# Optimization experiments

Hardware: AMD Instinct MI355X
Metric: run time of the kernel (lower is better)

The kernel has to match this reference:

```python
import jax, jax.numpy as jnp
import numpy as np

DIM = 768
H = 12          # num_heads
KV = 4          # kv_heads
D = DIM // H    # head_dim = 64
ROPE_BASE = 10000.0
WINDOW = 8
B, N = 4, 1024


def setup_inputs() -> dict:
    key = jax.random.key(0)
    ks = jax.random.split(key, 8)
    s = 0.02  # weight scale for sane magnitudes
    return {
        "x": jax.random.normal(ks[0], (B, N, DIM), jnp.float32),
        "Wq": jax.random.normal(ks[1], (2 * DIM, DIM), jnp.float32) * s,
        "Wk": jax.random.normal(ks[2], (2 * DIM * KV // H, DIM), jnp.float32) * s,
        "Wv1": jax.random.normal(ks[3], (DIM * KV // H, DIM), jnp.float32) * s,
        "Wv2": jax.random.normal(ks[4], (DIM * KV // H, DIM), jnp.float32) * s,
        "lambda_p": jnp.full((H, 1, 1), -2.0, jnp.float32),
        "Wo": jax.random.normal(ks[5], (DIM, DIM), jnp.float32) * s,
        "bo": jax.random.normal(ks[6], (DIM,), jnp.float32) * s,
    }


def _rotate_half(x):
    x1 = x[..., ::2]
    x2 = x[..., 1::2]
    return jnp.stack([-x2, x1], axis=-1).reshape(x.shape)


def _rope_cos_sin(n, dtype):
    side = int(n ** 0.5)
    if side * side == n:
        h = np.arange(side, dtype=np.float32)
        gh, gw = np.meshgrid(h, h, indexing="ij")
        pos_h, pos_w = gh.reshape(-1), gw.reshape(-1)
    else:
        pos_h = np.arange(n, dtype=np.float32)
        pos_w = np.zeros_like(pos_h)
    dim_half = D // 2
    inv_freq = ROPE_BASE ** (-np.arange(dim_half, dtype=np.float32) / dim_half)
    theta = np.concatenate([pos_h[:, None] * inv_freq[None, :],
                            pos_w[:, None] * inv_freq[None, :]], axis=1)  # [N, D]
    cos = jnp.asarray(np.cos(theta), dtype)[None, None]  # [1,1,N,D]
    sin = jnp.asarray(np.sin(theta), dtype)[None, None]
    return cos, sin


def _apply_rope(q, cos, sin):
    return q * cos + _rotate_half(q) * sin


def _qk_norm(t):
    return t / (jnp.linalg.norm(t, axis=-1, keepdims=True) + 1e-6)


def _window_mask(n, dtype):
    side = int(n ** 0.5)
    if side * side == n:
        h = np.arange(side)
        gh, gw = np.meshgrid(h, h, indexing="ij")
        coords = np.stack([gh.reshape(-1), gw.reshape(-1)], axis=1)  # [N,2]
        dist = np.abs(coords[:, None, :] - coords[None, :, :]).max(-1)  # Chebyshev
    else:
        idx = np.arange(n)
        dist = np.abs(idx[None, :] - idx[:, None])
    return jnp.asarray(np.where(dist > WINDOW, -np.inf, 0.0).astype(np.float32), dtype)


def _attend(q, k, v, mask):
    # q,k,v: [B,H,N,D]; mask additive [N,N]
    scale = 1.0 / np.sqrt(D)
    scores = jnp.einsum("bhnd,bhmd->bhnm", q, k) * scale + mask
    return jnp.einsum("bhnm,bhmd->bhnd", jax.nn.softmax(scores, axis=-1), v)


def reference(x, Wq, Wk, Wv1, Wv2, lambda_p, Wo, bo):
    b, n, c = x.shape
    rep = H // KV
    q = (x @ Wq.T).reshape(b, n, 2, H, D).transpose(2, 0, 3, 1, 4)   # [2,B,H,N,D]
    k = (x @ Wk.T).reshape(b, n, 2, KV, D).transpose(2, 0, 3, 1, 4)  # [2,B,KV,N,D]
    v1 = (x @ Wv1.T).reshape(b, n, KV, D).transpose(0, 2, 1, 3)      # [B,KV,N,D]
    v2 = (x @ Wv2.T).reshape(b, n, KV, D).transpose(0, 2, 1, 3)
    q1, q2 = q[0], q[1]
    k1, k2 = k[0], k[1]
    # GQA: repeat_interleave over head axis
    k1 = jnp.repeat(k1, rep, axis=1)
    k2 = jnp.repeat(k2, rep, axis=1)
    v1 = jnp.repeat(v1, rep, axis=1)
    v2 = jnp.repeat(v2, rep, axis=1)
    cos, sin = _rope_cos_sin(n, x.dtype)
    q1, q2 = _apply_rope(q1, cos, sin), _apply_rope(q2, cos, sin)
    k1, k2 = _apply_rope(k1, cos, sin), _apply_rope(k2, cos, sin)
    q1, q2, k1, k2 = _qk_norm(q1), _qk_norm(q2), _qk_norm(k1), _qk_norm(k2)
    mask = _window_mask(n, x.dtype)
    out1 = _attend(q1, k1, v1, mask)
    out2 = _attend(q2, k2, v2, mask)
    lam = jax.nn.softplus(lambda_p)  # [H,1,1] broadcasts over [B,H,N,D]
    out = out1 - lam[None] * out2
    out = out.transpose(0, 2, 1, 3).reshape(b, n, c)
    return out @ Wo.T + bo
```

## Files before the change

### kernel.cpp

```cpp
#include <hip/hip_runtime.h>
#include <hip/hip_bf16.h>

#define BATCH 4
#define NSEQ  1024
#define DIM   768
#define NH    12
#define NKV   4
#define HD    64
#define NTOK  (BATCH*NSEQ)

using bf16 = __hip_bfloat16;
typedef __attribute__((ext_vector_type(8))) short short8;
typedef __attribute__((ext_vector_type(4))) float floatx4;

__device__ __forceinline__ float b2f(short x) {
  unsigned u = ((unsigned)(unsigned short)x) << 16;
  return __builtin_bit_cast(float, u);
}
__device__ __forceinline__ unsigned short f2b(float f) {
  unsigned u = __builtin_bit_cast(unsigned, f);
  unsigned r = u + 0x7FFF + ((u >> 16) & 1);
  return (unsigned short)(r >> 16);
}

__device__ __forceinline__ void load_lds_16(const bf16* g, bf16* l) {
  __builtin_amdgcn_global_load_lds(
      (const __attribute__((address_space(1))) void*)g,
      (__attribute__((address_space(3))) void*)l, 16, 0, 0);
}

__global__ __launch_bounds__(256) void cvt_all(
    const float* __restrict__ x,  const float* __restrict__ wq,
    const float* __restrict__ wk, const float* __restrict__ wv1,
    const float* __restrict__ wv2, const float* __restrict__ wo,
    bf16* __restrict__ xb,  bf16* __restrict__ wqb, bf16* __restrict__ wkb,
    bf16* __restrict__ wv1b, bf16* __restrict__ wv2b, bf16* __restrict__ wob)
{
  int i = blockIdx.x * 256 + threadIdx.x;
  const float* s; bf16* d; int off;
  if      (i <  786432) { s = x;   d = xb;   off = i; }
  else if (i < 1081344) { s = wq;  d = wqb;  off = i -  786432; }
  else if (i < 1179648) { s = wk;  d = wkb;  off = i - 1081344; }
  else if (i < 1228800) { s = wv1; d = wv1b; off = i - 1179648; }
  else if (i < 1277952) { s = wv2; d = wv2b; off = i - 1228800; }
  else                  { s = wo;  d = wob;  off = i - 1277952; }
  float4 f = reinterpret_cast<const float4*>(s)[off];
  ushort4 u;
  u.x = f2b(f.x); u.y = f2b(f.y); u.z = f2b(f.z); u.w = f2b(f.w);
  reinterpret_cast<ushort4*>(d)[off] = u;
}

__global__ __launch_bounds__(256, 2) void gemm_qkv(
    const bf16* __restrict__ xb,
    const bf16* __restrict__ Wqb, const bf16* __restrict__ Wkb,
    const bf16* __restrict__ Wv1b, const bf16* __restrict__ Wv2b,
    bf16* __restrict__ Qpk, bf16* __restrict__ Kpk,
    bf16* __restrict__ Vpk1, bf16* __restrict__ Vpk2)
{
  __shared__ __align__(16) bf16 As[128 * 32];
  __shared__ __align__(16) bf16 Ws[128 * 32];

  const int bn = blockIdx.x, bm = blockIdx.y;
  const bf16* Wp;
  if (bn < 12)      Wp = Wqb  + (size_t)bn * 128 * 768;
  else if (bn < 16) Wp = Wkb  + (size_t)(bn - 12) * 128 * 768;
  else if (bn < 18) Wp = Wv1b + (size_t)(bn - 16) * 128 * 768;
  else              Wp = Wv2b + (size_t)(bn - 18) * 128 * 768;

  const int t = threadIdx.x, wave = t >> 6, lane = t & 63;
  const int wm = wave >> 1, wn = wave & 1;
  const int quad = lane >> 4, lr = lane & 15;

  const int srow = wave * 32 + (lane >> 2);
  const int scol = (lane & 3) * 8;
  const bf16* Ag = xb + (size_t)(bm * 128 + srow) * 768 + scol;
  const bf16* Wg = Wp + (size_t)srow * 768 + scol;
  bf16* Al0 = As + wave * 1024;
  bf16* Al1 = As + wave * 1024 + 512;
  bf16* Wl0 = Ws + wave * 1024;
  bf16* Wl1 = Ws + wave * 1024 + 512;

  floatx4 acc[4][4] = {};

  for (int k0 = 0; k0 < 768; k0 += 32) {
    load_lds_16(Ag + k0,            Al0);
    load_lds_16(Ag + 16 * 768 + k0, Al1);
    load_lds_16(Wg + k0,            Wl0);
    load_lds_16(Wg + 16 * 768 + k0, Wl1);
    __syncthreads();

    short8 af[4], wf[4];
    #pragma unroll
    for (int mt = 0; mt < 4; ++mt)
      af[mt] = *reinterpret_cast<const short8*>(&As[(wm * 64 + mt * 16 + lr) * 32 + quad * 8]);
    #pragma unroll
    for (int nt = 0; nt < 4; ++nt)
      wf[nt] = *reinterpret_cast<const short8*>(&Ws[(wn * 64 + nt * 16 + lr) * 32 + quad * 8]);

    #pragma unroll
    for (int mt = 0; mt < 4; ++mt)
      #pragma unroll
      for (int nt = 0; nt < 4; ++nt)
        acc[mt][nt] = __builtin_amdgcn_mfma_f32_16x16x32_bf16(af[mt], wf[nt], acc[mt][nt], 0, 0, 0);
    __syncthreads();
  }

  if (bn < 16) {
    const float K2 = 0.41524101186098309f;
    const float invf0 = exp2f(-(float)lr * K2);
    const float invf1 = exp2f(-(float)(16 + lr) * K2);
    const float sgn = (lr & 1) ? 1.f : -1.f;
    const bool isq = (bn < 12);
    const int hq = bn * 2 + wn;
    const int sq_ = hq / 12, hq_ = hq % 12;
    const int hh = (bn - 12) * 2 + wn;
    const int sk_ = hh >> 2, kvh_ = hh & 3;
    const int qk128 = (lr >> 3) * 128;
    #pragma unroll
    for (int mt = 0; mt < 4; ++mt) {
      #pragma unroll
      for (int r = 0; r < 4; ++r) {
        int row = bm * 128 + wm * 64 + mt * 16 + quad * 4 + r;
        int n = row & (NSEQ - 1);
        float ph = (float)(n >> 5), pw = (float)(n & 31);
        float v0 = acc[mt][0][r];
        float v1 = acc[mt][1][r];
        float v2 = acc[mt][2][r];
        float v3 = acc[mt][3][r];
        float rot0 = sgn * __shfl_xor(v0, 1);
        float rot1 = sgn * __shfl_xor(v1, 1);
        float rot2 = sgn * __shfl_xor(v2, 1);
        float rot3 = sgn * __shfl_xor(v3, 1);
        float t0 = ph * invf0, t1 = ph * invf1, t2 = pw * invf0, t3 = pw * invf1;
        float rv0 = v0 * __cosf(t0) + rot0 * __sinf(t0);
        float rv1 = v1 * __cosf(t1) + rot1 * __sinf(t1);
        float rv2 = v2 * __cosf(t2) + rot2 * __sinf(t2);
        float rv3 = v3 * __cosf(t3) + rot3 * __sinf(t3);
        float ss = rv0 * rv0 + rv1 * rv1 + rv2 * rv2 + rv3 * rv3;
        #pragma unroll
        for (int off = 1; off < 16; off <<= 1) ss += __shfl_xor(ss, off);
        float sc = 1.f / (sqrtf(ss) + 1e-6f);
        int bb = row >> 10, kh = n >> 5;
        size_t fo = (size_t)(mt & 1) * 1024 + (quad * 4 + r) * 8 + (lr & 7) + qk128;
        bf16* tb;
        if (isq) {
          tb = Qpk + ((size_t)((bb * 2 + sq_) * 12 + hq_) * 32 + kh) * 2048 + fo;
        } else {
          tb = Kpk + ((size_t)((bb * 2 + sk_) * 4 + kvh_) * 32 + kh) * 2048 + fo;
        }
        *(unsigned short*)&tb[0]   = f2b(rv0 * sc);
        *(unsigned short*)&tb[256] = f2b(rv1 * sc);
        *(unsigned short*)&tb[512] = f2b(rv2 * sc);
        *(unsigned short*)&tb[768] = f2b(rv3 * sc);
      }
    }
  } else {
    const bool is2 = (bn >= 18);
    bf16* Vp = is2 ? Vpk2 : Vpk1;
    const int kvh_ = (bn - (is2 ? 18 : 16)) * 2 + wn;
    #pragma unroll
    for (int mt = 0; mt < 4; ++mt)
      #pragma unroll
      for (int r = 0; r < 4; ++r) {
        int row = bm * 128 + wm * 64 + mt * 16 + quad * 4 + r;
        int n = row & (NSEQ - 1);
        int bb = row >> 10, kh = n >> 5;
        int rowm = (mt & 1) * 16 + quad * 4 + r;
        int quad_v = rowm >> 3, j = rowm & 7;
        bf16* tb = Vp + ((size_t)(bb * 4 + kvh_) * 32 + kh) * 2048
                   + quad_v * 128 + lr * 8 + j;
        *(unsigned short*)&tb[0]    = f2b(acc[mt][0][r]);
        *(unsigned short*)&tb[512]  = f2b(acc[mt][1][r]);
        *(unsigned short*)&tb[1024] = f2b(acc[mt][2][r]);
        *(unsigned short*)&tb[1536] = f2b(acc[mt][3][r]);
      }
  }
}

__global__ __launch_bounds__(256) void gemm_out(
    const bf16* __restrict__ Xb, const bf16* __restrict__ Wob,
    float* __restrict__ out, const float* __restrict__ bias)
{
  __shared__ __align__(16) bf16 As[64 * 32];
  __shared__ __align__(16) bf16 Ws[64 * 32];

  const int bn = blockIdx.x, bm = blockIdx.y;
  const int t = threadIdx.x, wave = t >> 6, lane = t & 63;
  const int wm = wave >> 1, wn = wave & 1;
  const int quad = lane >> 4, lr = lane & 15;

  const int srow = wave * 16 + (lane >> 2);
  const int scol = (lane & 3) * 8;
  const bf16* Ag = Xb  + (size_t)(bm * 64 + srow) * 768 + scol;
  const bf16* Wg = Wob + (size_t)(bn * 64 + srow) * 768 + scol;
  bf16* Al = As + wave * 512;
  bf16* Wl = Ws + wave * 512;

  floatx4 acc[2][2] = {};

  for (int k0 = 0; k0 < 768; k0 += 32) {
    load_lds_16(Ag + k0, Al);
    load_lds_16(Wg + k0, Wl);
    __syncthreads();

    short8 af[2], wf[2];
    #pragma unroll
    for (int mt = 0; mt < 2; ++mt)
      af[mt] = *reinterpret_cast<const short8*>(&As[(wm * 32 + mt * 16 + lr) * 32 + quad * 8]);
    #pragma unroll
    for (int nt = 0; nt < 2; ++nt)
      wf[nt] = *reinterpret_cast<const short8*>(&Ws[(wn * 32 + nt * 16 + lr) * 32 + quad * 8]);

    #pragma unroll
    for (int mt = 0; mt < 2; ++mt)
      #pragma unroll
      for (int nt = 0; nt < 2; ++nt)
        acc[mt][nt] = __builtin_amdgcn_mfma_f32_16x16x32_bf16(af[mt], wf[nt], acc[mt][nt], 0, 0, 0);
    __syncthreads();
  }

  #pragma unroll
  for (int nt = 0; nt < 2; ++nt) {
    int col = bn * 64 + wn * 32 + nt * 16 + lr;
    float bv = bias[col];
    #pragma unroll
    for (int mt = 0; mt < 2; ++mt)
      #pragma unroll
      for (int r = 0; r < 4; ++r) {
        int row = bm * 64 + wm * 32 + mt * 16 + quad * 4 + r;
        out[(size_t)row * 768 + col] = acc[mt][nt][r] + bv;
      }
  }
}

struct Frag { short8 kf[2][2]; short8 vf[4]; };

__device__ __forceinline__ void attn_load(
    Frag& f, const bf16* __restrict__ kp, const bf16* __restrict__ vp,
    int kh, int lane8)
{
  const bf16* kt = kp + (size_t)kh * 2048 + lane8;
  const bf16* vt = vp + (size_t)kh * 2048 + lane8;
  f.kf[0][0] = *reinterpret_cast<const short8*>(kt);
  f.kf[0][1] = *reinterpret_cast<const short8*>(kt + 512);
  f.kf[1][0] = *reinterpret_cast<const short8*>(kt + 1024);
  f.kf[1][1] = *reinterpret_cast<const short8*>(kt + 1536);
  f.vf[0] = *reinterpret_cast<const short8*>(vt);
  f.vf[1] = *reinterpret_cast<const short8*>(vt + 512);
  f.vf[2] = *reinterpret_cast<const short8*>(vt + 1024);
  f.vf[3] = *reinterpret_cast<const short8*>(vt + 1536);
}

__device__ __forceinline__ void attn_step(
    const short8 (&qf)[2][2], const Frag& f, unsigned maskbits,
    floatx4 (&O)[2][4], float (&psum)[2][4], bf16* __restrict__ Pl,
    int quad, int lr)
{
  floatx4 S[2][2] = {};
  #pragma unroll
  for (int ks = 0; ks < 2; ++ks) {
    S[0][0] = __builtin_amdgcn_mfma_f32_16x16x32_bf16(qf[0][ks], f.kf[0][ks], S[0][0], 0, 0, 0);
    S[0][1] = __builtin_amdgcn_mfma_f32_16x16x32_bf16(qf[0][ks], f.kf[1][ks], S[0][1], 0, 0, 0);
    S[1][0] = __builtin_amdgcn_mfma_f32_16x16x32_bf16(qf[1][ks], f.kf[0][ks], S[1][0], 0, 0, 0);
    S[1][1] = __builtin_amdgcn_mfma_f32_16x16x32_bf16(qf[1][ks], f.kf[1][ks], S[1][1], 0, 0, 0);
  }

  #pragma unroll
  for (int mt = 0; mt < 2; ++mt)
    #pragma unroll
    for (int nt = 0; nt < 2; ++nt)
      #pragma unroll
      for (int r = 0; r < 4; ++r) {
        float p = __expf(S[mt][nt][r] * 0.125f);
        p = ((maskbits >> (mt * 8 + nt * 4 + r)) & 1u) ? p : 0.0f;
        psum[mt][r] += p;
        *(unsigned short*)&Pl[(mt * 16 + quad * 4 + r) * 40 + nt * 16 + lr] = f2b(p);
      }

  short8 pf0 = *reinterpret_cast<const short8*>(&Pl[(lr) * 40 + quad * 8]);
  short8 pf1 = *reinterpret_cast<const short8*>(&Pl[(16 + lr) * 40 + quad * 8]);
  #pragma unroll
  for (int ntd = 0; ntd < 4; ++ntd) {
    O[0][ntd] = __builtin_amdgcn_mfma_f32_16x16x32_bf16(pf0, f.vf[ntd], O[0][ntd], 0, 0, 0);
    O[1][ntd] = __builtin_amdgcn_mfma_f32_16x16x32_bf16(pf1, f.vf[ntd], O[1][ntd], 0, 0, 0);
  }
}

__global__ __launch_bounds__(256, 2) void attn_mfma(
    const bf16* __restrict__ Qpk, const bf16* __restrict__ Kpk,
    const bf16* __restrict__ Vpk1, const bf16* __restrict__ Vpk2,
    const float* __restrict__ lambda_p, bf16* __restrict__ X)
{
  __shared__ __align__(16) char smem[12800];

  const int bid = blockIdx.x;
  const int qh = bid & 31;
  const int hb = bid >> 5;
  const int h  = hb % 12;
  const int b  = hb / 12;
  const int kvh = h / 3;

  const int t = threadIdx.x;
  const int w = t >> 6;
  const int s = w >> 1;
  const int half = w & 1;
  const int lane = t & 63;
  const int quad = lane >> 4, lr = lane & 15;
  const int lane8 = lane * 8;

  bf16* Pl = (bf16*)(smem + w * 2560);
  float* Oslab = (float*)smem;
  float* Pslab = (float*)(smem + 8192);
  bf16* Xs = (bf16*)(smem + 8192);

  const int tok0 = b * NSEQ + qh * 32;

  short8 qf[2][2];
  {
    const bf16* qt = Qpk + ((size_t)((b * 2 + s) * 12 + h) * 32 + qh) * 2048 + lane8;
    qf[0][0] = *reinterpret_cast<const short8*>(qt);
    qf[0][1] = *reinterpret_cast<const short8*>(qt + 512);
    qf[1][0] = *reinterpret_cast<const short8*>(qt + 1024);
    qf[1][1] = *reinterpret_cast<const short8*>(qt + 1536);
  }

  unsigned maskbits = 0;
  #pragma unroll
  for (int mt = 0; mt < 2; ++mt)
    #pragma unroll
    for (int nt = 0; nt < 2; ++nt)
      #pragma unroll
      for (int r = 0; r < 4; ++r) {
        int qq = mt * 16 + quad * 4 + r;
        int km = nt * 16 + lr;
        int d = km - qq; if (d < 0) d = -d;
        if (d <= 8) maskbits |= 1u << (mt * 8 + nt * 4 + r);
      }

  floatx4 O[2][4] = {};
  float psum[2][4] = {};

  const int kh0 = (qh > 8) ? qh - 8 : 0;
  const int kh1 = (qh < 23) ? qh + 8 : 31;
  const int cnt = kh1 - kh0 + 1;
  const int cA = (cnt + 1) >> 1;
  const int khA = half ? kh0 + cA : kh0;
  const int khB = half ? kh1 : kh0 + cA - 1;

  const bf16* kpbase = Kpk + (size_t)((b * 2 + s) * 4 + kvh) * 32 * 2048;
  const bf16* vpbase = (s ? Vpk2 : Vpk1) + (size_t)(b * 4 + kvh) * 32 * 2048;

  Frag fA, fB;
  attn_load(fA, kpbase, vpbase, khA, lane8);
  attn_load(fB, kpbase, vpbase, (khA + 1 <= khB) ? khA + 1 : khB, lane8);

  int i = khA;
  while (true) {
    attn_step(qf, fA, maskbits, O, psum, Pl, quad, lr);
    if (i == khB) break;
    ++i;
    attn_load(fA, kpbase, vpbase, (i + 1 <= khB) ? i + 1 : i, lane8);
    attn_step(qf, fB, maskbits, O, psum, Pl, quad, lr);
    if (i == khB) break;
    ++i;
    attn_load(fB, kpbase, vpbase, (i + 1 <= khB) ? i + 1 : i, lane8);
  }

  auto writeslab = [&]() {
    #pragma unroll
    for (int mt = 0; mt < 2; ++mt)
      #pragma unroll
      for (int ntd = 0; ntd < 4; ++ntd)
        *reinterpret_cast<floatx4*>(&Oslab[(mt * 4 + ntd) * 256 + lane * 4]) = O[mt][ntd];
    floatx4 p0, p1;
    p0[0] = psum[0][0]; p0[1] = psum[0][1]; p0[2] = psum[0][2]; p0[3] = psum[0][3];
    p1[0] = psum[1][0]; p1[1] = psum[1][1]; p1[2] = psum[1][2]; p1[3] = psum[1][3];
    *reinterpret_cast<floatx4*>(&Pslab[lane * 4])       = p0;
    *reinterpret_cast<floatx4*>(&Pslab[256 + lane * 4]) = p1;
  };
  auto readadd_norm = [&]() {
    #pragma unroll
    for (int mt = 0; mt < 2; ++mt)
      #pragma unroll
      for (int ntd = 0; ntd < 4; ++ntd)
        O[mt][ntd] += *reinterpret_cast<const floatx4*>(&Oslab[(mt * 4 + ntd) * 256 + lane * 4]);
    floatx4 p0 = *reinterpret_cast<const floatx4*>(&Pslab[lane * 4]);
    floatx4 p1 = *reinterpret_cast<const floatx4*>(&Pslab[256 + lane * 4]);
    #pragma unroll
    for (int r = 0; r < 4; ++r) { psum[0][r] += p0[r]; psum[1][r] += p1[r]; }
    #pragma unroll
    for (int off = 1; off < 16; off <<= 1)
      #pragma unroll
      for (int mt = 0; mt < 2; ++mt)
        #pragma unroll
        for (int r = 0; r < 4; ++r)
          psum[mt][r] += __shfl_xor(psum[mt][r], off);
    #pragma unroll
    for (int mt = 0; mt < 2; ++mt)
      #pragma unroll
      for (int r = 0; r < 4; ++r)
        psum[mt][r] = 1.f / psum[mt][r];
    #pragma unroll
    for (int mt = 0; mt < 2; ++mt)
      #pragma unroll
      for (int ntd = 0; ntd < 4; ++ntd)
        #pragma unroll
        for (int r = 0; r < 4; ++r)
          O[mt][ntd][r] *= psum[mt][r];
  };

  __syncthreads();
  if (w == 1) writeslab();
  __syncthreads();
  if (w == 0) readadd_norm();
  __syncthreads();
  if (w == 3) writeslab();
  __syncthreads();
  if (w == 2) {
    readadd_norm();
    #pragma unroll
    for (int mt = 0; mt < 2; ++mt)
      #pragma unroll
      for (int ntd = 0; ntd < 4; ++ntd)
        *reinterpret_cast<floatx4*>(&Oslab[(mt * 4 + ntd) * 256 + lane * 4]) = O[mt][ntd];
  }
  __syncthreads();
  if (w == 0) {
    float lam = log1pf(__expf(lambda_p[h]));
    #pragma unroll
    for (int mt = 0; mt < 2; ++mt)
      #pragma unroll
      for (int ntd = 0; ntd < 4; ++ntd) {
        floatx4 o2 = *reinterpret_cast<const floatx4*>(&Oslab[(mt * 4 + ntd) * 256 + lane * 4]);
        #pragma unroll
        for (int r = 0; r < 4; ++r) {
          float xv = O[mt][ntd][r] - lam * o2[r];
          *(unsigned short*)&Xs[(mt * 16 + quad * 4 + r) * 72 + ntd * 16 + lr] = f2b(xv);
        }
      }
  }
  __syncthreads();

  {
    int row = t >> 3, seg = t & 7;
    short8 xv = *reinterpret_cast<const short8*>(&Xs[row * 72 + seg * 8]);
    *reinterpret_cast<short8*>(X + (size_t)(tok0 + row) * 768 + h * 64 + seg * 8) = xv;
  }
}

extern "C" void kernel_launch(void* const* d_in, const int* in_sizes, int n_in,
                              void* d_out, int out_size, void* d_ws, size_t ws_size,
                              hipStream_t stream)
{
  const float* x        = (const float*)d_in[0];
  const float* Wq       = (const float*)d_in[1];
  const float* Wk       = (const float*)d_in[2];
  const float* Wv1      = (const float*)d_in[3];
  const float* Wv2      = (const float*)d_in[4];
  const float* lambda_p = (const float*)d_in[5];
  const float* Wo       = (const float*)d_in[6];
  const float* bo       = (const float*)d_in[7];
  float* out = (float*)d_out;

  bf16* xb   = (bf16*)d_ws;
  bf16* Wqb  = xb   + (size_t)NTOK * 768;
  bf16* Wkb  = Wqb  + (size_t)1536 * 768;
  bf16* Wv1b = Wkb  + (size_t)512 * 768;
  bf16* Wv2b = Wv1b + (size_t)256 * 768;
  bf16* Wob  = Wv2b + (size_t)256 * 768;
  bf16* Qpk  = Wob  + (size_t)768 * 768;
  bf16* Xb   = Qpk  + (size_t)NTOK * 1536;
  bf16* Vpk1 = Xb   + (size_t)NTOK * 768;
  bf16* Vpk2 = Vpk1 + (size_t)512 * 2048;
  bf16* Kpk  = Vpk2 + (size_t)512 * 2048;

  cvt_all<<<5568, 256, 0, stream>>>(x, Wq, Wk, Wv1, Wv2, Wo,
                                    xb, Wqb, Wkb, Wv1b, Wv2b, Wob);

  gemm_qkv<<<dim3(20, 32), 256, 0, stream>>>(xb, Wqb, Wkb, Wv1b, Wv2b,
                                             Qpk, Kpk, Vpk1, Vpk2);

  attn_mfma<<<BATCH * NH * 32, 256, 0, stream>>>(Qpk, Kpk, Vpk1, Vpk2, lambda_p, Xb);

  gemm_out<<<dim3(12, 64), 256, 0, stream>>>(Xb, Wob, out, bo);
}
```

Baseline: 159.1 us.

## Fold softmax scale into Q, use exp2, packed bf16 converts, parallel slab reduce

The QK projection epilogue hoists the height-dependent RoPE sin/cos out of the row loop and multiplies normalized Q by scale*log2(e), so attention can use raw exp2 without a per-element multiply. Float-to-bf16 rounding now uses the packed v_cvt_pk_bf16_f32 instruction instead of the manual bit-twiddling. The cross-wave output reduction gets two separate LDS slabs so both query streams reduce in parallel, removing two barriers at the cost of more shared memory per block. Folding the scale into bf16 Q slightly changes rounding.

```diff
diff --git a/kernel.cpp b/kernel.cpp
--- a/kernel.cpp
+++ b/kernel.cpp
@@ -21,6 +21,11 @@
   unsigned u = __builtin_bit_cast(unsigned, f);
   unsigned r = u + 0x7FFF + ((u >> 16) & 1);
   return (unsigned short)(r >> 16);
+}
+__device__ __forceinline__ unsigned cvtpk(float lo, float hi) {
+  unsigned r;
+  asm("v_cvt_pk_bf16_f32 %0, %1, %2" : "=v"(r) : "v"(lo), "v"(hi));
+  return r;
 }
 
 __device__ __forceinline__ void load_lds_16(const bf16* g, bf16* l) {
@@ -118,11 +123,24 @@
     const int qk128 = (lr >> 3) * 128;
     #pragma unroll
     for (int mt = 0; mt < 4; ++mt) {
+      const int row0 = bm * 128 + wm * 64 + mt * 16 + quad * 4;
+      const int n0 = row0 & (NSEQ - 1);
+      const int bb = row0 >> 10, kh = n0 >> 5;
+      const float ph = (float)kh;
+      const float pw0 = (float)(n0 & 31);
+      const float t0 = ph * invf0, t1 = ph * invf1;
+      const float c0 = __cosf(t0), s0 = __sinf(t0);
+      const float c1 = __cosf(t1), s1 = __sinf(t1);
+      bf16* tb0;
+      if (isq) {
+        tb0 = Qpk + ((size_t)((bb * 2 + sq_) * 12 + hq_) * 32 + kh) * 2048
+              + (size_t)(mt & 1) * 1024 + qk128 + (quad * 4) * 8 + (lr & 7);
+      } else {
+        tb0 = Kpk + ((size_t)((bb * 2 + sk_) * 4 + kvh_) * 32 + kh) * 2048
+              + (size_t)(mt & 1) * 1024 + qk128 + (quad * 4) * 8 + (lr & 7);
+      }
       #pragma unroll
       for (int r = 0; r < 4; ++r) {
-        int row = bm * 128 + wm * 64 + mt * 16 + quad * 4 + r;
-        int n = row & (NSEQ - 1);
-        float ph = (float)(n >> 5), pw = (float)(n & 31);
         float v0 = acc[mt][0][r];
         float v1 = acc[mt][1][r];
         float v2 = acc[mt][2][r];
@@ -131,27 +149,24 @@
         float rot1 = sgn * __shfl_xor(v1, 1);
         float rot2 = sgn * __shfl_xor(v2, 1);
         float rot3 = sgn * __shfl_xor(v3, 1);
-        float t0 = ph * invf0, t1 = ph * invf1, t2 = pw * invf0, t3 = pw * invf1;
-        float rv0 = v0 * __cosf(t0) + rot0 * __sinf(t0);
-        float rv1 = v1 * __cosf(t1) + rot1 * __sinf(t1);
+        float pw = pw0 + (float)r;
+        float t2 = pw * invf0, t3 = pw * invf1;
+        float rv0 = v0 * c0 + rot0 * s0;
+        float rv1 = v1 * c1 + rot1 * s1;
         float rv2 = v2 * __cosf(t2) + rot2 * __sinf(t2);
         float rv3 = v3 * __cosf(t3) + rot3 * __sinf(t3);
         float ss = rv0 * rv0 + rv1 * rv1 + rv2 * rv2 + rv3 * rv3;
         #pragma unroll
         for (int off = 1; off < 16; off <<= 1) ss += __shfl_xor(ss, off);
         float sc = 1.f / (sqrtf(ss) + 1e-6f);
-        int bb = row >> 10, kh = n >> 5;
-        size_t fo = (size_t)(mt & 1) * 1024 + (quad * 4 + r) * 8 + (lr & 7) + qk128;
-        bf16* tb;
-        if (isq) {
-          tb = Qpk + ((size_t)((bb * 2 + sq_) * 12 + hq_) * 32 + kh) * 2048 + fo;
-        } else {
-          tb = Kpk + ((size_t)((bb * 2 + sk_) * 4 + kvh_) * 32 + kh) * 2048 + fo;
-        }
-        *(unsigned short*)&tb[0]   = f2b(rv0 * sc);
-        *(unsigned short*)&tb[256] = f2b(rv1 * sc);
-        *(unsigned short*)&tb[512] = f2b(rv2 * sc);
-        *(unsigned short*)&tb[768] = f2b(rv3 * sc);
+        if (isq) sc *= 0.18033688011112042f;
+        bf16* tb = tb0 + r * 8;
+        unsigned pkA = cvtpk(rv0 * sc, rv1 * sc);
+        unsigned pkB = cvtpk(rv2 * sc, rv3 * sc);
+        *(unsigned short*)&tb[0]   = (unsigned short)pkA;
+        *(unsigned short*)&tb[256] = (unsigned short)(pkA >> 16);
+        *(unsigned short*)&tb[512] = (unsigned short)pkB;
+        *(unsigned short*)&tb[768] = (unsigned short)(pkB >> 16);
       }
     }
   } else {
@@ -169,10 +184,12 @@
         int quad_v = rowm >> 3, j = rowm & 7;
         bf16* tb = Vp + ((size_t)(bb * 4 + kvh_) * 32 + kh) * 2048
                    + quad_v * 128 + lr * 8 + j;
-        *(unsigned short*)&tb[0]    = f2b(acc[mt][0][r]);
-        *(unsigned short*)&tb[512]  = f2b(acc[mt][1][r]);
-        *(unsigned short*)&tb[1024] = f2b(acc[mt][2][r]);
-        *(unsigned short*)&tb[1536] = f2b(acc[mt][3][r]);
+        unsigned pkA = cvtpk(acc[mt][0][r], acc[mt][1][r]);
+        unsigned pkB = cvtpk(acc[mt][2][r], acc[mt][3][r]);
+        *(unsigned short*)&tb[0]    = (unsigned short)pkA;
+        *(unsigned short*)&tb[512]  = (unsigned short)(pkA >> 16);
+        *(unsigned short*)&tb[1024] = (unsigned short)pkB;
+        *(unsigned short*)&tb[1536] = (unsigned short)(pkB >> 16);
       }
   }
 }
@@ -268,14 +285,23 @@
   #pragma unroll
   for (int mt = 0; mt < 2; ++mt)
     #pragma unroll
-    for (int nt = 0; nt < 2; ++nt)
+    for (int nt = 0; nt < 2; ++nt) {
+      float pr[4];
       #pragma unroll
       for (int r = 0; r < 4; ++r) {
-        float p = __expf(S[mt][nt][r] * 0.125f);
+        float p = __builtin_amdgcn_exp2f(S[mt][nt][r]);
         p = ((maskbits >> (mt * 8 + nt * 4 + r)) & 1u) ? p : 0.0f;
         psum[mt][r] += p;
-        *(unsigned short*)&Pl[(mt * 16 + quad * 4 + r) * 40 + nt * 16 + lr] = f2b(p);
-      }
+        pr[r] = p;
+      }
+      unsigned pkA = cvtpk(pr[0], pr[1]);
+      unsigned pkB = cvtpk(pr[2], pr[3]);
+      unsigned short* bp = (unsigned short*)&Pl[(mt * 16 + quad * 4) * 40 + nt * 16 + lr];
+      bp[0]   = (unsigned short)pkA;
+      bp[40]  = (unsigned short)(pkA >> 16);
+      bp[80]  = (unsigned short)pkB;
+      bp[120] = (unsigned short)(pkB >> 16);
+    }
 
   short8 pf0 = *reinterpret_cast<const short8*>(&Pl[(lr) * 40 + quad * 8]);
   short8 pf1 = *reinterpret_cast<const short8*>(&Pl[(16 + lr) * 40 + quad * 8]);
@@ -291,7 +317,7 @@
     const bf16* __restrict__ Vpk1, const bf16* __restrict__ Vpk2,
     const float* __restrict__ lambda_p, bf16* __restrict__ X)
 {
-  __shared__ __align__(16) char smem[12800];
+  __shared__ __align__(16) char smem[20480];
 
   const int bid = blockIdx.x;
   const int qh = bid & 31;
@@ -309,9 +335,9 @@
   const int lane8 = lane * 8;
 
   bf16* Pl = (bf16*)(smem + w * 2560);
-  float* Oslab = (float*)smem;
-  float* Pslab = (float*)(smem + 8192);
-  bf16* Xs = (bf16*)(smem + 8192);
+  float* myO = (float*)(smem + (s ? 10240 : 0));
+  float* myP = (float*)(smem + (s ? 10240 : 0) + 8192);
+  bf16* Xs = (bf16*)smem;
 
   const int tok0 = b * NSEQ + qh * 32;
 
@@ -371,21 +397,21 @@
     for (int mt = 0; mt < 2; ++mt)
       #pragma unroll
       for (int ntd = 0; ntd < 4; ++ntd)
-        *reinterpret_cast<floatx4*>(&Oslab[(mt * 4 + ntd) * 256 + lane * 4]) = O[mt][ntd];
+        *reinterpret_cast<floatx4*>(&myO[(mt * 4 + ntd) * 256 + lane * 4]) = O[mt][ntd];
     floatx4 p0, p1;
     p0[0] = psum[0][0]; p0[1] = psum[0][1]; p0[2] = psum[0][2]; p0[3] = psum[0][3];
     p1[0] = psum[1][0]; p1[1] = psum[1][1]; p1[2] = psum[1][2]; p1[3] = psum[1][3];
-    *reinterpret_cast<floatx4*>(&Pslab[lane * 4])       = p0;
-    *reinterpret_cast<floatx4*>(&Pslab[256 + lane * 4]) = p1;
+    *reinterpret_cast<floatx4*>(&myP[lane * 4])       = p0;
+    *reinterpret_cast<floatx4*>(&myP[256 + lane * 4]) = p1;
   };
   auto readadd_norm = [&]() {
     #pragma unroll
     for (int mt = 0; mt < 2; ++mt)
       #pragma unroll
       for (int ntd = 0; ntd < 4; ++ntd)
-        O[mt][ntd] += *reinterpret_cast<const floatx4*>(&Oslab[(mt * 4 + ntd) * 256 + lane * 4]);
-    floatx4 p0 = *reinterpret_cast<const floatx4*>(&Pslab[lane * 4]);
-    floatx4 p1 = *reinterpret_cast<const floatx4*>(&Pslab[256 + lane * 4]);
+        O[mt][ntd] += *reinterpret_cast<const floatx4*>(&myO[(mt * 4 + ntd) * 256 + lane * 4]);
+    floatx4 p0 = *reinterpret_cast<const floatx4*>(&myP[lane * 4]);
+    floatx4 p1 = *reinterpret_cast<const floatx4*>(&myP[256 + lane * 4]);
     #pragma unroll
     for (int r = 0; r < 4; ++r) { psum[0][r] += p0[r]; psum[1][r] += p1[r]; }
     #pragma unroll
@@ -410,28 +436,27 @@
   };
 
   __syncthreads();
-  if (w == 1) writeslab();
+  if (half) writeslab();
   __syncthreads();
-  if (w == 0) readadd_norm();
-  __syncthreads();
-  if (w == 3) writeslab();
-  __syncthreads();
-  if (w == 2) {
+  if (!half) {
     readadd_norm();
-    #pragma unroll
-    for (int mt = 0; mt < 2; ++mt)
-      #pragma unroll
-      for (int ntd = 0; ntd < 4; ++ntd)
-        *reinterpret_cast<floatx4*>(&Oslab[(mt * 4 + ntd) * 256 + lane * 4]) = O[mt][ntd];
+    if (s) {
+      #pragma unroll
+      for (int mt = 0; mt < 2; ++mt)
+        #pragma unroll
+        for (int ntd = 0; ntd < 4; ++ntd)
+          *reinterpret_cast<floatx4*>(&myO[(mt * 4 + ntd) * 256 + lane * 4]) = O[mt][ntd];
+    }
   }
   __syncthreads();
   if (w == 0) {
+    const float* O2s = (const float*)(smem + 10240);
     float lam = log1pf(__expf(lambda_p[h]));
     #pragma unroll
     for (int mt = 0; mt < 2; ++mt)
       #pragma unroll
       for (int ntd = 0; ntd < 4; ++ntd) {
-        floatx4 o2 = *reinterpret_cast<const floatx4*>(&Oslab[(mt * 4 + ntd) * 256 + lane * 4]);
+        floatx4 o2 = *reinterpret_cast<const floatx4*>(&O2s[(mt * 4 + ntd) * 256 + lane * 4]);
         #pragma unroll
         for (int r = 0; r < 4; ++r) {
           float xv = O[mt][ntd][r] - lam * o2[r];
```

Measured after the change: 154.4 us. 1.03x faster.
